# Optimization experiments

Hardware: AMD Instinct MI355X
Metric: run time of the kernel (lower is better)

## Reference

```python
import jax, jax.numpy as jnp
import numpy as np

THETA = 0.5


def setup_inputs() -> dict:
    key = jax.random.key(0)
    k1, k2 = jax.random.split(key)
    N = 8388608
    predicted = jax.random.normal(k1, (N,), dtype=jnp.float32)
    labels = jax.random.normal(k2, (N,), dtype=jnp.float32)
    return {"predicted": predicted, "labels": labels}


def reference(predicted, labels):
    diff = predicted - labels
    # branchless asymmetric scoring: exp(-d/13)-1 if d<0 else exp(d/10)-1, summed
    scoring = jnp.sum(
        jnp.where(diff < 0, jnp.exp(-diff / 13.0), jnp.exp(diff / 10.0)) - 1.0
    )
    rmse = jnp.sqrt(jnp.mean(diff * diff))
    return THETA * scoring + (1.0 - THETA) * rmse
```

## Files before the change

kernel.cpp:

```cpp
#include <hip/hip_runtime.h>
#include <math.h>

constexpr int BLOCKS  = 1024;
constexpr int THREADS = 256;
constexpr int WAVES   = THREADS / 64;

__device__ __forceinline__ void score_accum(float4 p, float4 l,
                                            float& sc, float& sq) {
    const float cneg = -1.0f / 13.0f;
    const float cpos =  1.0f / 10.0f;
    float d0 = p.x - l.x, d1 = p.y - l.y, d2 = p.z - l.z, d3 = p.w - l.w;
    float t0 = d0 * (d0 < 0.0f ? cneg : cpos);
    float t1 = d1 * (d1 < 0.0f ? cneg : cpos);
    float t2 = d2 * (d2 < 0.0f ? cneg : cpos);
    float t3 = d3 * (d3 < 0.0f ? cneg : cpos);
    sc += (__expf(t0) - 1.0f) + (__expf(t1) - 1.0f)
        + (__expf(t2) - 1.0f) + (__expf(t3) - 1.0f);
    sq += d0 * d0 + d1 * d1 + d2 * d2 + d3 * d3;
}

__device__ __forceinline__ void block_reduce_store(float sc, float sq,
                                                   float* partials) {
    #pragma unroll
    for (int off = 32; off > 0; off >>= 1) {
        sc += __shfl_down(sc, off, 64);
        sq += __shfl_down(sq, off, 64);
    }
    __shared__ float s_sc[WAVES];
    __shared__ float s_sq[WAVES];
    const int lane = threadIdx.x & 63;
    const int wave = threadIdx.x >> 6;
    if (lane == 0) { s_sc[wave] = sc; s_sq[wave] = sq; }
    __syncthreads();
    if (threadIdx.x == 0) {
        float tsc = 0.0f, tsq = 0.0f;
        #pragma unroll
        for (int w = 0; w < WAVES; ++w) { tsc += s_sc[w]; tsq += s_sq[w]; }
        partials[blockIdx.x]          = tsc;
        partials[BLOCKS + blockIdx.x] = tsq;
    }
}

template <int ITERS>
__global__ __launch_bounds__(THREADS)
void rul_partial_fixed(const float* __restrict__ pred,
                       const float* __restrict__ lab,
                       float* __restrict__ partials) {
    const float4* __restrict__ p4 = reinterpret_cast<const float4*>(pred);
    const float4* __restrict__ l4 = reinterpret_cast<const float4*>(lab);
    const int stride = BLOCKS * THREADS;
    const int base   = blockIdx.x * THREADS + threadIdx.x;

    float4 p[ITERS], l[ITERS];
    #pragma unroll
    for (int k = 0; k < ITERS; ++k) p[k] = p4[base + k * stride];
    #pragma unroll
    for (int k = 0; k < ITERS; ++k) l[k] = l4[base + k * stride];

    float sc = 0.0f, sq = 0.0f;
    #pragma unroll
    for (int k = 0; k < ITERS; ++k) score_accum(p[k], l[k], sc, sq);

    block_reduce_store(sc, sq, partials);
}

__global__ __launch_bounds__(THREADS)
void rul_partial_generic(const float* __restrict__ pred,
                         const float* __restrict__ lab,
                         float* __restrict__ partials, int n) {
    const float4* __restrict__ p4 = reinterpret_cast<const float4*>(pred);
    const float4* __restrict__ l4 = reinterpret_cast<const float4*>(lab);
    const int n4 = n >> 2;
    float sc = 0.0f, sq = 0.0f;
    for (int i = blockIdx.x * THREADS + threadIdx.x; i < n4;
         i += gridDim.x * THREADS) {
        score_accum(p4[i], l4[i], sc, sq);
    }
    block_reduce_store(sc, sq, partials);
}

__global__ __launch_bounds__(THREADS)
void rul_final(const float* __restrict__ partials,
               float* __restrict__ out, int n) {
    float sc = 0.0f, sq = 0.0f;
    for (int i = threadIdx.x; i < BLOCKS; i += THREADS) {
        sc += partials[i];
        sq += partials[BLOCKS + i];
    }
    #pragma unroll
    for (int off = 32; off > 0; off >>= 1) {
        sc += __shfl_down(sc, off, 64);
        sq += __shfl_down(sq, off, 64);
    }
    __shared__ float s_sc[WAVES];
    __shared__ float s_sq[WAVES];
    const int lane = threadIdx.x & 63;
    const int wave = threadIdx.x >> 6;
    if (lane == 0) { s_sc[wave] = sc; s_sq[wave] = sq; }
    __syncthreads();
    if (threadIdx.x == 0) {
        float tsc = 0.0f, tsq = 0.0f;
        #pragma unroll
        for (int w = 0; w < WAVES; ++w) { tsc += s_sc[w]; tsq += s_sq[w]; }
        out[0] = 0.5f * tsc + 0.5f * sqrtf(tsq / (float)n);
    }
}

extern "C" void kernel_launch(void* const* d_in, const int* in_sizes, int n_in,
                              void* d_out, int out_size, void* d_ws, size_t ws_size,
                              hipStream_t stream) {
    const float* pred = (const float*)d_in[0];
    const float* lab  = (const float*)d_in[1];
    const int n = in_sizes[0];
    float* partials = (float*)d_ws;

    if (n == BLOCKS * THREADS * 8 * 4) {
        rul_partial_fixed<8><<<BLOCKS, THREADS, 0, stream>>>(pred, lab, partials);
    } else {
        rul_partial_generic<<<BLOCKS, THREADS, 0, stream>>>(pred, lab, partials, n);
    }
    rul_final<<<1, THREADS, 0, stream>>>(partials, (float*)d_out, n);
}
```

Measured before the change: 92.27 us.

## Fuse final reduction into partial kernel via last-block atomic counter

Replaces the separate single-block final reduction kernel with a last-block-done pattern: each block writes its partial sums, fences, and increments an atomic counter, and the last block reduces all partials and writes the result. This is meant to remove a second kernel launch and the gap between launches. In exchange it adds a hipMemsetAsync of the counter on every call, an atomic and fences per block, and a serial tail handled by one block.

```diff
diff --git a/kernel.cpp b/kernel.cpp
--- a/kernel.cpp
+++ b/kernel.cpp
@@ -19,8 +19,7 @@
     sq += d0 * d0 + d1 * d1 + d2 * d2 + d3 * d3;
 }
 
-__device__ __forceinline__ void block_reduce_store(float sc, float sq,
-                                                   float* partials) {
+__device__ __forceinline__ void block_reduce(float& sc, float& sq) {
     #pragma unroll
     for (int off = 32; off > 0; off >>= 1) {
         sc += __shfl_down(sc, off, 64);
@@ -36,73 +35,62 @@
         float tsc = 0.0f, tsq = 0.0f;
         #pragma unroll
         for (int w = 0; w < WAVES; ++w) { tsc += s_sc[w]; tsq += s_sq[w]; }
-        partials[blockIdx.x]          = tsc;
-        partials[BLOCKS + blockIdx.x] = tsq;
+        sc = tsc; sq = tsq;
     }
 }
 
-template <int ITERS>
+template <bool FIXED>
 __global__ __launch_bounds__(THREADS)
-void rul_partial_fixed(const float* __restrict__ pred,
-                       const float* __restrict__ lab,
-                       float* __restrict__ partials) {
+void rul_fused(const float* __restrict__ pred,
+               const float* __restrict__ lab,
+               float2* __restrict__ partials,
+               unsigned int* __restrict__ counter,
+               float* __restrict__ out, int n) {
     const float4* __restrict__ p4 = reinterpret_cast<const float4*>(pred);
     const float4* __restrict__ l4 = reinterpret_cast<const float4*>(lab);
-    const int stride = BLOCKS * THREADS;
-    const int base   = blockIdx.x * THREADS + threadIdx.x;
-
-    float4 p[ITERS], l[ITERS];
-    #pragma unroll
-    for (int k = 0; k < ITERS; ++k) p[k] = p4[base + k * stride];
-    #pragma unroll
-    for (int k = 0; k < ITERS; ++k) l[k] = l4[base + k * stride];
 
     float sc = 0.0f, sq = 0.0f;
-    #pragma unroll
-    for (int k = 0; k < ITERS; ++k) score_accum(p[k], l[k], sc, sq);
+    if (FIXED) {
+        constexpr int ITERS = 8;
+        const int stride = BLOCKS * THREADS;
+        const int base   = blockIdx.x * THREADS + threadIdx.x;
+        float4 p[ITERS], l[ITERS];
+        #pragma unroll
+        for (int k = 0; k < ITERS; ++k) p[k] = p4[base + k * stride];
+        #pragma unroll
+        for (int k = 0; k < ITERS; ++k) l[k] = l4[base + k * stride];
+        #pragma unroll
+        for (int k = 0; k < ITERS; ++k) score_accum(p[k], l[k], sc, sq);
+    } else {
+        const int n4 = n >> 2;
+        for (int i = blockIdx.x * THREADS + threadIdx.x; i < n4;
+             i += gridDim.x * THREADS) {
+            score_accum(p4[i], l4[i], sc, sq);
+        }
+    }
 
-    block_reduce_store(sc, sq, partials);
-}
+    block_reduce(sc, sq);
 
-__global__ __launch_bounds__(THREADS)
-void rul_partial_generic(const float* __restrict__ pred,
-                         const float* __restrict__ lab,
-                         float* __restrict__ partials, int n) {
-    const float4* __restrict__ p4 = reinterpret_cast<const float4*>(pred);
-    const float4* __restrict__ l4 = reinterpret_cast<const float4*>(lab);
-    const int n4 = n >> 2;
-    float sc = 0.0f, sq = 0.0f;
-    for (int i = blockIdx.x * THREADS + threadIdx.x; i < n4;
-         i += gridDim.x * THREADS) {
-        score_accum(p4[i], l4[i], sc, sq);
+    __shared__ bool is_last;
+    if (threadIdx.x == 0) {
+        partials[blockIdx.x] = make_float2(sc, sq);
+        __threadfence();
+        unsigned int old = atomicAdd(counter, 1u);
+        is_last = (old == gridDim.x - 1);
     }
-    block_reduce_store(sc, sq, partials);
-}
+    __syncthreads();
 
-__global__ __launch_bounds__(THREADS)
-void rul_final(const float* __restrict__ partials,
-               float* __restrict__ out, int n) {
-    float sc = 0.0f, sq = 0.0f;
-    for (int i = threadIdx.x; i < BLOCKS; i += THREADS) {
-        sc += partials[i];
-        sq += partials[BLOCKS + i];
-    }
-    #pragma unroll
-    for (int off = 32; off > 0; off >>= 1) {
-        sc += __shfl_down(sc, off, 64);
-        sq += __shfl_down(sq, off, 64);
-    }
-    __shared__ float s_sc[WAVES];
-    __shared__ float s_sq[WAVES];
-    const int lane = threadIdx.x & 63;
-    const int wave = threadIdx.x >> 6;
-    if (lane == 0) { s_sc[wave] = sc; s_sq[wave] = sq; }
-    __syncthreads();
-    if (threadIdx.x == 0) {
-        float tsc = 0.0f, tsq = 0.0f;
-        #pragma unroll
-        for (int w = 0; w < WAVES; ++w) { tsc += s_sc[w]; tsq += s_sq[w]; }
-        out[0] = 0.5f * tsc + 0.5f * sqrtf(tsq / (float)n);
+    if (is_last) {
+        __threadfence();
+        float fsc = 0.0f, fsq = 0.0f;
+        for (int i = threadIdx.x; i < gridDim.x; i += THREADS) {
+            float2 v = partials[i];
+            fsc += v.x; fsq += v.y;
+        }
+        block_reduce(fsc, fsq);
+        if (threadIdx.x == 0) {
+            out[0] = 0.5f * fsc + 0.5f * sqrtf(fsq / (float)n);
+        }
     }
 }
 
@@ -112,12 +100,17 @@
     const float* pred = (const float*)d_in[0];
     const float* lab  = (const float*)d_in[1];
     const int n = in_sizes[0];
-    float* partials = (float*)d_ws;
+
+    unsigned int* counter = (unsigned int*)d_ws;
+    float2* partials = (float2*)((char*)d_ws + 256);
+
+    hipMemsetAsync(counter, 0, sizeof(unsigned int), stream);
 
     if (n == BLOCKS * THREADS * 8 * 4) {
-        rul_partial_fixed<8><<<BLOCKS, THREADS, 0, stream>>>(pred, lab, partials);
+        rul_fused<true><<<BLOCKS, THREADS, 0, stream>>>(
+            pred, lab, partials, counter, (float*)d_out, n);
     } else {
-        rul_partial_generic<<<BLOCKS, THREADS, 0, stream>>>(pred, lab, partials, n);
+        rul_fused<false><<<BLOCKS, THREADS, 0, stream>>>(
+            pred, lab, partials, counter, (float*)d_out, n);
     }
-    rul_final<<<1, THREADS, 0, stream>>>(partials, (float*)d_out, n);
 }
```

New measurement: 125.8 us. 36.3% more time.
